# Optimization experiments

Hardware: AMD Instinct MI355X
Metric: run time of the kernel (lower is better)

Reference implementation:

```python
import jax, jax.numpy as jnp
import numpy as np

N, E, F_IN, H, C = 20000, 320000, 256, 4, 64
D = H * C  # hidden_dim = 256
NEG_SLOPE = 0.2
LN_EPS = 1e-5


def setup_inputs() -> dict:
    key = jax.random.key(0)
    ks = jax.random.split(key, 12)
    x = jax.random.normal(ks[0], (N, F_IN), dtype=jnp.float32)
    # edges guaranteed self-loop-free (PyG GATConv removes then re-adds self loops)
    dst = jax.random.randint(ks[1], (E,), 0, N)
    off = jax.random.randint(ks[2], (E,), 1, N)
    src = (dst + off) % N
    edge_index = jnp.stack([src, dst]).astype(jnp.int64)

    def lin(k, fan_in, shape):
        return jax.random.normal(k, shape, dtype=jnp.float32) / np.sqrt(fan_in)

    W1 = lin(ks[3], F_IN, (F_IN, D)); b1 = jnp.zeros((D,), jnp.float32)
    a_src1 = lin(ks[4], C, (H, C)); a_dst1 = lin(ks[5], C, (H, C))
    W2 = lin(ks[6], D, (D, D)); b2 = jnp.zeros((D,), jnp.float32)
    a_src2 = lin(ks[7], C, (H, C)); a_dst2 = lin(ks[8], C, (H, C))
    g1 = jnp.ones((D,), jnp.float32); be1 = jnp.zeros((D,), jnp.float32)
    g2 = jnp.ones((D,), jnp.float32); be2 = jnp.zeros((D,), jnp.float32)
    attn_w = lin(ks[9], D, (D, 1)); attn_b = jnp.zeros((1,), jnp.float32)
    return dict(x=x, edge_index=edge_index, W1=W1, b1=b1, a_src1=a_src1,
                a_dst1=a_dst1, W2=W2, b2=b2, a_src2=a_src2, a_dst2=a_dst2,
                g1=g1, be1=be1, g2=g2, be2=be2, attn_w=attn_w, attn_b=attn_b)


def _gat_conv(x, src, dst, W, b, a_src, a_dst):
    # x: [N, F] -> h: [N, H, C]
    h = (x @ W).reshape(N, H, C)
    alpha_s = jnp.einsum('nhc,hc->nh', h, a_src)  # [N, H]
    alpha_d = jnp.einsum('nhc,hc->nh', h, a_dst)
    e = jax.nn.leaky_relu(alpha_s[src] + alpha_d[dst], NEG_SLOPE)  # [E', H]
    # segment softmax over edges sharing a destination
    m = jax.ops.segment_max(e, dst, num_segments=N)
    w = jnp.exp(e - m[dst])
    z = jax.ops.segment_sum(w, dst, num_segments=N)
    alpha = w / (z[dst] + 1e-16)
    out = jax.ops.segment_sum(h[src] * alpha[:, :, None], dst, num_segments=N)
    return out.reshape(N, D) + b


def _layernorm(x, g, b):
    mu = x.mean(-1, keepdims=True)
    var = ((x - mu) ** 2).mean(-1, keepdims=True)
    return (x - mu) * jax.lax.rsqrt(var + LN_EPS) * g + b


def reference(x, edge_index, W1, b1, a_src1, a_dst1, W2, b2, a_src2, a_dst2,
              g1, be1, g2, be2, attn_w, attn_b):
    loops = jnp.arange(N, dtype=edge_index.dtype)
    src = jnp.concatenate([edge_index[0], loops])
    dst = jnp.concatenate([edge_index[1], loops])
    x1 = _gat_conv(x, src, dst, W1, b1, a_src1, a_dst1)
    x1 = jax.nn.elu(_layernorm(x1, g1, be1))
    x2 = _gat_conv(x1, src, dst, W2, b2, a_src2, a_dst2)
    x2 = jax.nn.elu(_layernorm(x2, g2, be2) + x1)
    attn = jax.nn.softmax(x2 @ attn_w + attn_b, axis=0)  # softmax over nodes
    pooled = (x2 * attn).sum(axis=0)  # [D]
    return pooled
```

## Files before the change

kernel.cpp:

```cpp
#include <hip/hip_runtime.h>
#include <math.h>

#define N_NODES 20000
#define E_EDGES 320000
#define TOT_E   (E_EDGES + N_NODES)
#define DHID    256
#define NHEAD   4
#define SCAN_NB ((N_NODES + 255) / 256)
#define SPART   32
#define ECAP    128
#define EB_K    ((TOT_E + 255) / 256)
#define XB_K    (N_NODES * 256 / 8 / 256)

typedef float f32x4 __attribute__((ext_vector_type(4)));
typedef short short8 __attribute__((ext_vector_type(8)));
typedef unsigned short ushort;

__device__ __forceinline__ float wave_sum(float v) {
#pragma unroll
  for (int off = 32; off; off >>= 1) v += __shfl_xor(v, off);
  return v;
}
__device__ __forceinline__ ushort f2bf(float f) {
  unsigned u = __float_as_uint(f);
  u += 0x7fffu + ((u >> 16) & 1u);
  return (ushort)(u >> 16);
}
__device__ __forceinline__ float bflo(unsigned u) {
  return __uint_as_float(u << 16);
}
__device__ __forceinline__ float bfhi(unsigned u) {
  return __uint_as_float(u & 0xffff0000u);
}

__global__ __launch_bounds__(256)
void conv_hist_kernel(const float* __restrict__ W1, const float* __restrict__ W2,
                      const float* __restrict__ x, const int* __restrict__ ei,
                      ushort* __restrict__ Wt1, ushort* __restrict__ Wt2,
                      ushort* __restrict__ xb, int* __restrict__ deg) {
  const int b = blockIdx.x;
  if (b < 512) {
    const float* W = (b < 256) ? W1 : W2;
    ushort* Wt = (b < 256) ? Wt1 : Wt2;
    const int n = b & 255;
    const int k = threadIdx.x;
    Wt[n * 256 + k] = f2bf(W[k * 256 + n]);
  } else if (b < 512 + XB_K) {
    int idx = (b - 512) * 256 + threadIdx.x;
    size_t base = (size_t)idx * 8;
    float4 a = *reinterpret_cast<const float4*>(x + base);
    float4 c = *reinterpret_cast<const float4*>(x + base + 4);
    short8 o;
    o[0] = f2bf(a.x); o[1] = f2bf(a.y); o[2] = f2bf(a.z); o[3] = f2bf(a.w);
    o[4] = f2bf(c.x); o[5] = f2bf(c.y); o[6] = f2bf(c.z); o[7] = f2bf(c.w);
    *reinterpret_cast<short8*>(xb + base) = o;
  } else {
    int e = (b - 512 - XB_K) * 256 + threadIdx.x;
    if (e < TOT_E) {
      int dst = (e < E_EDGES) ? ei[E_EDGES + e] : (e - E_EDGES);
      atomicAdd(&deg[dst], 1);
    }
  }
}

__global__ __launch_bounds__(256)
void scan_blocks_kernel(const int* __restrict__ deg, int* __restrict__ bsum) {
  __shared__ int ws[4];
  const int t = threadIdx.x;
  const int i = blockIdx.x * 256 + t;
  int v = (i < N_NODES) ? deg[i] : 0;
  int s = v;
#pragma unroll
  for (int off = 32; off; off >>= 1) s += __shfl_xor(s, off);
  if ((t & 63) == 0) ws[t >> 6] = s;
  __syncthreads();
  if (t == 0) bsum[blockIdx.x] = ws[0] + ws[1] + ws[2] + ws[3];
}

__global__ __launch_bounds__(256)
void scan_apply_kernel(const int* __restrict__ deg, const int* __restrict__ bsum,
                       int* __restrict__ rowp, int* __restrict__ cur) {
  __shared__ int ws[4], ws2[4];
  const int t = threadIdx.x;
  const int lane = t & 63, w = t >> 6;
  int part = 0;
  for (int k = t; k < blockIdx.x; k += 256) part += bsum[k];
#pragma unroll
  for (int off = 32; off; off >>= 1) part += __shfl_xor(part, off);
  if (lane == 0) ws[w] = part;
  __syncthreads();
  const int boff = ws[0] + ws[1] + ws[2] + ws[3];
  const int i = blockIdx.x * 256 + t;
  int v = (i < N_NODES) ? deg[i] : 0;
  int inc = v;
#pragma unroll
  for (int off = 1; off < 64; off <<= 1) {
    int u = __shfl_up(inc, off);
    if (lane >= off) inc += u;
  }
  if (lane == 63) ws2[w] = inc;
  __syncthreads();
  int add = boff;
#pragma unroll
  for (int k = 0; k < 4; ++k)
    if (k < w) add += ws2[k];
  int exc = add + inc - v;
  if (i < N_NODES) {
    rowp[i] = exc;
    cur[i] = exc;
    if (i == N_NODES - 1) rowp[N_NODES] = exc + v;
  }
}

__global__ void scatter_kernel(const int* __restrict__ ei, int* __restrict__ cur,
                               int* __restrict__ colb) {
  int e = blockIdx.x * blockDim.x + threadIdx.x;
  if (e >= TOT_E) return;
  int src, dst;
  if (e < E_EDGES) { src = ei[e]; dst = ei[E_EDGES + e]; }
  else             { src = dst = e - E_EDGES; }
  int pos = atomicAdd(&cur[dst], 1);
  colb[pos] = src;
}

__global__ __launch_bounds__(256)
void gemm_alpha_kernel(const ushort* __restrict__ Ab, const ushort* __restrict__ Wt,
                       const float* __restrict__ asrc, const float* __restrict__ adst,
                       ushort* __restrict__ hout, float* __restrict__ as_,
                       float* __restrict__ ad_) {
  __shared__ ushort hs[32 * 256];

  const int t = threadIdx.x;
  const int w = t >> 6;
  const int l = t & 63;
  const int row0 = blockIdx.x * 32;

  const ushort* abase = Ab + (size_t)(row0 + (l & 15)) * 256 + ((l >> 4) * 8);
  const ushort* bbase = Wt + (size_t)(w * 64 + (l & 15)) * 256 + ((l >> 4) * 8);

  f32x4 acc[2][4];
#pragma unroll
  for (int i = 0; i < 2; ++i)
#pragma unroll
    for (int j = 0; j < 4; ++j) acc[i][j] = (f32x4){0.f, 0.f, 0.f, 0.f};

  short8 a0 = *reinterpret_cast<const short8*>(abase);
  short8 a1 = *reinterpret_cast<const short8*>(abase + 16 * 256);
  short8 b0 = *reinterpret_cast<const short8*>(bbase);
  short8 b1 = *reinterpret_cast<const short8*>(bbase + 16 * 256);
  short8 b2 = *reinterpret_cast<const short8*>(bbase + 32 * 256);
  short8 b3 = *reinterpret_cast<const short8*>(bbase + 48 * 256);
#pragma unroll
  for (int kk = 0; kk < 256; kk += 32) {
    short8 na0, na1, nb0, nb1, nb2, nb3;
    if (kk + 32 < 256) {
      na0 = *reinterpret_cast<const short8*>(abase + kk + 32);
      na1 = *reinterpret_cast<const short8*>(abase + 16 * 256 + kk + 32);
      nb0 = *reinterpret_cast<const short8*>(bbase + kk + 32);
      nb1 = *reinterpret_cast<const short8*>(bbase + 16 * 256 + kk + 32);
      nb2 = *reinterpret_cast<const short8*>(bbase + 32 * 256 + kk + 32);
      nb3 = *reinterpret_cast<const short8*>(bbase + 48 * 256 + kk + 32);
    }
    acc[0][0] = __builtin_amdgcn_mfma_f32_16x16x32_bf16(a0, b0, acc[0][0], 0, 0, 0);
    acc[0][1] = __builtin_amdgcn_mfma_f32_16x16x32_bf16(a0, b1, acc[0][1], 0, 0, 0);
    acc[0][2] = __builtin_amdgcn_mfma_f32_16x16x32_bf16(a0, b2, acc[0][2], 0, 0, 0);
    acc[0][3] = __builtin_amdgcn_mfma_f32_16x16x32_bf16(a0, b3, acc[0][3], 0, 0, 0);
    acc[1][0] = __builtin_amdgcn_mfma_f32_16x16x32_bf16(a1, b0, acc[1][0], 0, 0, 0);
    acc[1][1] = __builtin_amdgcn_mfma_f32_16x16x32_bf16(a1, b1, acc[1][1], 0, 0, 0);
    acc[1][2] = __builtin_amdgcn_mfma_f32_16x16x32_bf16(a1, b2, acc[1][2], 0, 0, 0);
    acc[1][3] = __builtin_amdgcn_mfma_f32_16x16x32_bf16(a1, b3, acc[1][3], 0, 0, 0);
    if (kk + 32 < 256) {
      a0 = na0; a1 = na1; b0 = nb0; b1 = nb1; b2 = nb2; b3 = nb3;
    }
  }

  float asj[4], adj[4];
#pragma unroll
  for (int j = 0; j < 4; ++j) {
    asj[j] = asrc[w * 64 + j * 16 + (l & 15)];
    adj[j] = adst[w * 64 + j * 16 + (l & 15)];
  }
#pragma unroll
  for (int i = 0; i < 2; ++i) {
#pragma unroll
    for (int q = 0; q < 4; ++q) {
      float ps = 0.f, pd = 0.f;
#pragma unroll
      for (int j = 0; j < 4; ++j) {
        ps += acc[i][j][q] * asj[j];
        pd += acc[i][j][q] * adj[j];
      }
#pragma unroll
      for (int off = 1; off < 16; off <<= 1) {
        ps += __shfl_xor(ps, off);
        pd += __shfl_xor(pd, off);
      }
      int row = row0 + i * 16 + (l >> 4) * 4 + q;
      if ((l & 15) == 0) {
        as_[row * 4 + w] = ps;
        ad_[row * 4 + w] = pd;
      }
    }
  }

#pragma unroll
  for (int i = 0; i < 2; ++i)
#pragma unroll
    for (int j = 0; j < 4; ++j)
#pragma unroll
      for (int q = 0; q < 4; ++q) {
        int row = i * 16 + (l >> 4) * 4 + q;
        int col = w * 64 + j * 16 + (l & 15);
        hs[row * 256 + col] = f2bf(acc[i][j][q]);
      }
  __syncthreads();
#pragma unroll
  for (int g = 0; g < 4; ++g) {
    int gi = g * 256 + t;
    int row = gi >> 5;
    int slot = gi & 31;
    *reinterpret_cast<short8*>(hout + (size_t)(row0 + row) * 256 + slot * 8) =
        *reinterpret_cast<const short8*>(&hs[row * 256 + slot * 8]);
  }
}

__global__ __launch_bounds__(256)
void attn_gather_ln_kernel(const ushort* __restrict__ h, const float* __restrict__ as_,
                           const float* __restrict__ ad_, const int* __restrict__ rowp,
                           const int* __restrict__ colb, const float* __restrict__ bias,
                           const float* __restrict__ gamma, const float* __restrict__ beta,
                           const ushort* __restrict__ residb, ushort* __restrict__ outb,
                           const float* __restrict__ aw, const float* __restrict__ ab,
                           float* __restrict__ score) {
  __shared__ float ew[4][ECAP][NHEAD];
  __shared__ int   sidx[4][ECAP];

  const int t = threadIdx.x;
  const int wd = t >> 6;
  const int d = blockIdx.x * 4 + wd;
  const int l = t & 63;
  const int start = rowp[d];
  const int deg = rowp[d + 1] - start;
  const int* cb = colb + start;

  const int e16 = l >> 2, hh = l & 3;
  const float adv = ad_[d * 4 + hh];
  const int gh = l >> 4;
  const int c0 = l * 4;
  const ushort* hrow = h + c0;

  float zpart = 0.f;
  float a0 = 0.f, a1 = 0.f, a2 = 0.f, a3 = 0.f;

  for (int base = 0; base < deg; base += ECAP) {
    const int cnt = min(deg - base, ECAP);
    for (int i = e16; i < cnt; i += 16) {
      int s = cb[base + i];
      if (hh == 0) sidx[wd][i] = s;
      float e = as_[s * 4 + hh] + adv;
      e = (e >= 0.f) ? e : 0.2f * e;
      e = fminf(e, 60.f);
      float wv = __expf(e);
      ew[wd][i][hh] = wv;
      zpart += wv;
    }
    int i = 0;
    for (; i + 8 <= cnt; i += 8) {
      int ss[8]; float ww[8]; uint2 hv[8];
#pragma unroll
      for (int k = 0; k < 8; ++k) { ss[k] = sidx[wd][i + k]; ww[k] = ew[wd][i + k][gh]; }
#pragma unroll
      for (int k = 0; k < 8; ++k)
        hv[k] = *reinterpret_cast<const uint2*>(hrow + (size_t)ss[k] * 256);
#pragma unroll
      for (int k = 0; k < 8; ++k) {
        a0 += ww[k] * bflo(hv[k].x); a1 += ww[k] * bfhi(hv[k].x);
        a2 += ww[k] * bflo(hv[k].y); a3 += ww[k] * bfhi(hv[k].y);
      }
    }
    for (; i + 4 <= cnt; i += 4) {
      int ss[4]; float ww[4]; uint2 hv[4];
#pragma unroll
      for (int k = 0; k < 4; ++k) { ss[k] = sidx[wd][i + k]; ww[k] = ew[wd][i + k][gh]; }
#pragma unroll
      for (int k = 0; k < 4; ++k)
        hv[k] = *reinterpret_cast<const uint2*>(hrow + (size_t)ss[k] * 256);
#pragma unroll
      for (int k = 0; k < 4; ++k) {
        a0 += ww[k] * bflo(hv[k].x); a1 += ww[k] * bfhi(hv[k].x);
        a2 += ww[k] * bflo(hv[k].y); a3 += ww[k] * bfhi(hv[k].y);
      }
    }
    for (; i < cnt; ++i) {
      int s = sidx[wd][i];
      float wv = ew[wd][i][gh];
      uint2 hv = *reinterpret_cast<const uint2*>(hrow + (size_t)s * 256);
      a0 += wv * bflo(hv.x);
      a1 += wv * bfhi(hv.x);
      a2 += wv * bflo(hv.y);
      a3 += wv * bfhi(hv.y);
    }
  }

#pragma unroll
  for (int off = 4; off < 64; off <<= 1) zpart += __shfl_xor(zpart, off);
  const float zi = 1.f / (__shfl(zpart, gh) + 1e-16f);

  float4 bi = *reinterpret_cast<const float4*>(bias + c0);
  float v0 = a0 * zi + bi.x, v1 = a1 * zi + bi.y;
  float v2 = a2 * zi + bi.z, v3 = a3 * zi + bi.w;

  float s1 = wave_sum(v0 + v1 + v2 + v3);
  float s2 = wave_sum(v0 * v0 + v1 * v1 + v2 * v2 + v3 * v3);
  float mu = s1 * (1.f / 256.f);
  float var = s2 * (1.f / 256.f) - mu * mu;
  float rstd = rsqrtf(var + 1e-5f);
  float4 ga = *reinterpret_cast<const float4*>(gamma + c0);
  float4 be = *reinterpret_cast<const float4*>(beta + c0);
  float y0 = (v0 - mu) * rstd * ga.x + be.x;
  float y1 = (v1 - mu) * rstd * ga.y + be.y;
  float y2 = (v2 - mu) * rstd * ga.z + be.z;
  float y3 = (v3 - mu) * rstd * ga.w + be.w;
  if (residb) {
    uint2 rv = *reinterpret_cast<const uint2*>(residb + (size_t)d * 256 + c0);
    y0 += bflo(rv.x); y1 += bfhi(rv.x); y2 += bflo(rv.y); y3 += bfhi(rv.y);
  }
  y0 = (y0 > 0.f) ? y0 : expm1f(y0);
  y1 = (y1 > 0.f) ? y1 : expm1f(y1);
  y2 = (y2 > 0.f) ? y2 : expm1f(y2);
  y3 = (y3 > 0.f) ? y3 : expm1f(y3);

  uint2 o;
  o.x = ((unsigned)f2bf(y0)) | (((unsigned)f2bf(y1)) << 16);
  o.y = ((unsigned)f2bf(y2)) | (((unsigned)f2bf(y3)) << 16);
  *reinterpret_cast<uint2*>(outb + (size_t)d * 256 + c0) = o;

  if (score) {
    float4 aww = *reinterpret_cast<const float4*>(aw + c0);
    float sp = wave_sum(y0 * aww.x + y1 * aww.y + y2 * aww.z + y3 * aww.w);
    if (l == 0) score[d] = sp + ab[0];
  }
}

__global__ __launch_bounds__(256)
void score_part_kernel(const float* __restrict__ s, float* __restrict__ pm,
                       float* __restrict__ pz) {
  __shared__ float red[4];
  const int t = threadIdx.x, b = blockIdx.x;
  const int lane = t & 63, wid = t >> 6;
  float m = -INFINITY;
  for (int n = b * 256 + t; n < N_NODES; n += SPART * 256) m = fmaxf(m, s[n]);
#pragma unroll
  for (int off = 32; off; off >>= 1) m = fmaxf(m, __shfl_xor(m, off));
  if (lane == 0) red[wid] = m;
  __syncthreads();
  m = fmaxf(fmaxf(red[0], red[1]), fmaxf(red[2], red[3]));
  __syncthreads();
  float z = 0.f;
  for (int n = b * 256 + t; n < N_NODES; n += SPART * 256) z += __expf(s[n] - m);
  z = wave_sum(z);
  if (lane == 0) red[wid] = z;
  __syncthreads();
  if (t == 0) { pm[b] = m; pz[b] = red[0] + red[1] + red[2] + red[3]; }
}

__global__ __launch_bounds__(64)
void score_comb_kernel(const float* __restrict__ pm, const float* __restrict__ pz,
                       float* __restrict__ mz) {
  const int l = threadIdx.x;
  float m = (l < SPART) ? pm[l] : -INFINITY;
#pragma unroll
  for (int off = 32; off; off >>= 1) m = fmaxf(m, __shfl_xor(m, off));
  float z = (l < SPART) ? pz[l] * __expf(pm[l] - m) : 0.f;
  z = wave_sum(z);
  if (l == 0) { mz[0] = m; mz[1] = z; }
}

__global__ __launch_bounds__(256)
void pool_partial_kernel(const ushort* __restrict__ hb2, const float* __restrict__ s,
                         const float* __restrict__ mz, float* __restrict__ part) {
  __shared__ float red4[4][256];
  const int t = threadIdx.x, b = blockIdx.x;
  const int c4 = t & 63, rsub = t >> 6;
  const float m = mz[0];
  const float invz = 1.f / mz[1];
  f32x4 acc = (f32x4){0.f, 0.f, 0.f, 0.f};
  for (int n = b * 4 + rsub; n < N_NODES; n += 1024) {
    float w = __expf(s[n] - m);
    uint2 hv = *reinterpret_cast<const uint2*>(hb2 + (size_t)n * 256 + c4 * 4);
    acc[0] += w * bflo(hv.x);
    acc[1] += w * bfhi(hv.x);
    acc[2] += w * bflo(hv.y);
    acc[3] += w * bfhi(hv.y);
  }
#pragma unroll
  for (int k = 0; k < 4; ++k) red4[rsub][c4 * 4 + k] = acc[k];
  __syncthreads();
  if (t < 256) {
    float v = red4[0][t] + red4[1][t] + red4[2][t] + red4[3][t];
    part[b * 256 + t] = v * invz;
  }
}

__global__ __launch_bounds__(256)
void pool_final_kernel(const float* __restrict__ part, float* __restrict__ out) {
  const int t = threadIdx.x;
  float acc = 0.f;
  for (int b = 0; b < 256; ++b) acc += part[b * 256 + t];
  out[t] = acc;
}

extern "C" void kernel_launch(void* const* d_in, const int* in_sizes, int n_in,
                              void* d_out, int out_size, void* d_ws, size_t ws_size,
                              hipStream_t stream) {
  const float* x      = (const float*)d_in[0];
  const int*   ei     = (const int*)d_in[1];
  const float* W1     = (const float*)d_in[2];
  const float* b1     = (const float*)d_in[3];
  const float* a_src1 = (const float*)d_in[4];
  const float* a_dst1 = (const float*)d_in[5];
  const float* W2     = (const float*)d_in[6];
  const float* b2     = (const float*)d_in[7];
  const float* a_src2 = (const float*)d_in[8];
  const float* a_dst2 = (const float*)d_in[9];
  const float* g1     = (const float*)d_in[10];
  const float* be1    = (const float*)d_in[11];
  const float* g2     = (const float*)d_in[12];
  const float* be2    = (const float*)d_in[13];
  const float* attn_w = (const float*)d_in[14];
  const float* attn_b = (const float*)d_in[15];
  float* out = (float*)d_out;

  char* p = (char*)d_ws;
  auto alloc = [&](size_t bytes) {
    char* r = p;
    p += (bytes + 255) & ~size_t(255);
    return r;
  };
  ushort* h   = (ushort*)alloc((size_t)N_NODES * 256 * 2);
  ushort* xb  = (ushort*)alloc((size_t)N_NODES * 256 * 2);
  ushort* xb1 = (ushort*)alloc((size_t)N_NODES * 256 * 2);
  ushort* hb2 = (ushort*)alloc((size_t)N_NODES * 256 * 2);
  float* as_  = (float*)alloc((size_t)N_NODES * 4 * 4);
  float* ad_  = (float*)alloc((size_t)N_NODES * 4 * 4);
  float* sbuf = (float*)alloc((size_t)N_NODES * 4);
  float* mz   = (float*)alloc(256);
  float* pm   = (float*)alloc((size_t)SPART * 4);
  float* pz   = (float*)alloc((size_t)SPART * 4);
  float* part = (float*)alloc((size_t)256 * 256 * 4);
  ushort* wt1 = (ushort*)alloc((size_t)256 * 256 * 2);
  ushort* wt2 = (ushort*)alloc((size_t)256 * 256 * 2);
  int* deg    = (int*)alloc((size_t)N_NODES * 4);
  int* rowp   = (int*)alloc((size_t)(N_NODES + 1) * 4);
  int* cur    = (int*)alloc((size_t)N_NODES * 4);
  int* colb   = (int*)alloc((size_t)TOT_E * 4);
  int* bsum   = (int*)alloc((size_t)SCAN_NB * 4);

  const int GB = N_NODES / 32;
  const int DB = N_NODES / 4;
  const int CONVB = 512 + XB_K + EB_K;

  hipMemsetAsync(deg, 0, (size_t)N_NODES * 4, stream);
  conv_hist_kernel<<<CONVB, 256, 0, stream>>>(W1, W2, x, ei, wt1, wt2, xb, deg);
  scan_blocks_kernel<<<SCAN_NB, 256, 0, stream>>>(deg, bsum);
  scan_apply_kernel<<<SCAN_NB, 256, 0, stream>>>(deg, bsum, rowp, cur);
  scatter_kernel<<<EB_K, 256, 0, stream>>>(ei, cur, colb);

  gemm_alpha_kernel<<<GB, 256, 0, stream>>>(xb, wt1, a_src1, a_dst1, h, as_, ad_);
  attn_gather_ln_kernel<<<DB, 256, 0, stream>>>(h, as_, ad_, rowp, colb, b1, g1, be1,
                                                nullptr, xb1, nullptr, nullptr, nullptr);
  gemm_alpha_kernel<<<GB, 256, 0, stream>>>(xb1, wt2, a_src2, a_dst2, h, as_, ad_);
  attn_gather_ln_kernel<<<DB, 256, 0, stream>>>(h, as_, ad_, rowp, colb, b2, g2, be2,
                                                xb1, hb2, attn_w, attn_b, sbuf);
  score_part_kernel<<<SPART, 256, 0, stream>>>(sbuf, pm, pz);
  score_comb_kernel<<<1, 64, 0, stream>>>(pm, pz, mz);
  pool_partial_kernel<<<256, 256, 0, stream>>>(hb2, sbuf, mz, part);
  pool_final_kernel<<<1, 256, 0, stream>>>(part, out);
}
```

Measured before the change: 173.0 us.

## Prescale gather offsets, raise wave priority in gather loop, fuse score combine into pool

The gather kernel now stores source indices pre-shifted into byte offsets in shared memory, which removes the per-edge multiply from the address calculation. It also raises wave priority with s_setprio around the gather loop so waves issuing loads get scheduled first. The separate single-block score_comb kernel is removed; each pool_partial block recomputes the global max and normalizer from the 32 partials, which saves one launch at the cost of redundant tiny work in every block. The shifted offset s<<9 stays within int range for 20000 nodes.

```diff
diff --git a/kernel.cpp b/kernel.cpp
--- a/kernel.cpp
+++ b/kernel.cpp
@@ -247,7 +247,7 @@
   const float adv = ad_[d * 4 + hh];
   const int gh = l >> 4;
   const int c0 = l * 4;
-  const ushort* hrow = h + c0;
+  const char* hrow = reinterpret_cast<const char*>(h + c0);
 
   float zpart = 0.f;
   float a0 = 0.f, a1 = 0.f, a2 = 0.f, a3 = 0.f;
@@ -256,7 +256,7 @@
     const int cnt = min(deg - base, ECAP);
     for (int i = e16; i < cnt; i += 16) {
       int s = cb[base + i];
-      if (hh == 0) sidx[wd][i] = s;
+      if (hh == 0) sidx[wd][i] = s << 9;
       float e = as_[s * 4 + hh] + adv;
       e = (e >= 0.f) ? e : 0.2f * e;
       e = fminf(e, 60.f);
@@ -264,6 +264,7 @@
       ew[wd][i][hh] = wv;
       zpart += wv;
     }
+    __builtin_amdgcn_s_setprio(1);
     int i = 0;
     for (; i + 8 <= cnt; i += 8) {
       int ss[8]; float ww[8]; uint2 hv[8];
@@ -271,7 +272,7 @@
       for (int k = 0; k < 8; ++k) { ss[k] = sidx[wd][i + k]; ww[k] = ew[wd][i + k][gh]; }
 #pragma unroll
       for (int k = 0; k < 8; ++k)
-        hv[k] = *reinterpret_cast<const uint2*>(hrow + (size_t)ss[k] * 256);
+        hv[k] = *reinterpret_cast<const uint2*>(hrow + (size_t)ss[k]);
 #pragma unroll
       for (int k = 0; k < 8; ++k) {
         a0 += ww[k] * bflo(hv[k].x); a1 += ww[k] * bfhi(hv[k].x);
@@ -284,7 +285,7 @@
       for (int k = 0; k < 4; ++k) { ss[k] = sidx[wd][i + k]; ww[k] = ew[wd][i + k][gh]; }
 #pragma unroll
       for (int k = 0; k < 4; ++k)
-        hv[k] = *reinterpret_cast<const uint2*>(hrow + (size_t)ss[k] * 256);
+        hv[k] = *reinterpret_cast<const uint2*>(hrow + (size_t)ss[k]);
 #pragma unroll
       for (int k = 0; k < 4; ++k) {
         a0 += ww[k] * bflo(hv[k].x); a1 += ww[k] * bfhi(hv[k].x);
@@ -292,14 +293,15 @@
       }
     }
     for (; i < cnt; ++i) {
-      int s = sidx[wd][i];
+      int soff = sidx[wd][i];
       float wv = ew[wd][i][gh];
-      uint2 hv = *reinterpret_cast<const uint2*>(hrow + (size_t)s * 256);
+      uint2 hv = *reinterpret_cast<const uint2*>(hrow + (size_t)soff);
       a0 += wv * bflo(hv.x);
       a1 += wv * bfhi(hv.x);
       a2 += wv * bflo(hv.y);
       a3 += wv * bfhi(hv.y);
     }
+    __builtin_amdgcn_s_setprio(0);
   }
 
 #pragma unroll
@@ -364,26 +366,25 @@
   if (t == 0) { pm[b] = m; pz[b] = red[0] + red[1] + red[2] + red[3]; }
 }
 
-__global__ __launch_bounds__(64)
-void score_comb_kernel(const float* __restrict__ pm, const float* __restrict__ pz,
-                       float* __restrict__ mz) {
-  const int l = threadIdx.x;
-  float m = (l < SPART) ? pm[l] : -INFINITY;
-#pragma unroll
-  for (int off = 32; off; off >>= 1) m = fmaxf(m, __shfl_xor(m, off));
-  float z = (l < SPART) ? pz[l] * __expf(pm[l] - m) : 0.f;
-  z = wave_sum(z);
-  if (l == 0) { mz[0] = m; mz[1] = z; }
-}
-
 __global__ __launch_bounds__(256)
 void pool_partial_kernel(const ushort* __restrict__ hb2, const float* __restrict__ s,
-                         const float* __restrict__ mz, float* __restrict__ part) {
+                         const float* __restrict__ pm, const float* __restrict__ pz,
+                         float* __restrict__ part) {
   __shared__ float red4[4][256];
+  __shared__ float sMZ[2];
   const int t = threadIdx.x, b = blockIdx.x;
   const int c4 = t & 63, rsub = t >> 6;
-  const float m = mz[0];
-  const float invz = 1.f / mz[1];
+  if (t < 64) {
+    float m = (t < SPART) ? pm[t] : -INFINITY;
+#pragma unroll
+    for (int off = 32; off; off >>= 1) m = fmaxf(m, __shfl_xor(m, off));
+    float z = (t < SPART) ? pz[t] * __expf(pm[t] - m) : 0.f;
+    z = wave_sum(z);
+    if (t == 0) { sMZ[0] = m; sMZ[1] = z; }
+  }
+  __syncthreads();
+  const float m = sMZ[0];
+  const float invz = 1.f / sMZ[1];
   f32x4 acc = (f32x4){0.f, 0.f, 0.f, 0.f};
   for (int n = b * 4 + rsub; n < N_NODES; n += 1024) {
     float w = __expf(s[n] - m);
@@ -444,7 +445,6 @@
   float* as_  = (float*)alloc((size_t)N_NODES * 4 * 4);
   float* ad_  = (float*)alloc((size_t)N_NODES * 4 * 4);
   float* sbuf = (float*)alloc((size_t)N_NODES * 4);
-  float* mz   = (float*)alloc(256);
   float* pm   = (float*)alloc((size_t)SPART * 4);
   float* pz   = (float*)alloc((size_t)SPART * 4);
   float* part = (float*)alloc((size_t)256 * 256 * 4);
@@ -473,7 +473,6 @@
   attn_gather_ln_kernel<<<DB, 256, 0, stream>>>(h, as_, ad_, rowp, colb, b2, g2, be2,
                                                 xb1, hb2, attn_w, attn_b, sbuf);
   score_part_kernel<<<SPART, 256, 0, stream>>>(sbuf, pm, pz);
-  score_comb_kernel<<<1, 64, 0, stream>>>(pm, pz, mz);
-  pool_partial_kernel<<<256, 256, 0, stream>>>(hb2, sbuf, mz, part);
+  pool_partial_kernel<<<256, 256, 0, stream>>>(hb2, sbuf, pm, pz, part);
   pool_final_kernel<<<1, 256, 0, stream>>>(part, out);
 }
```

Result: no change. 174.2 us (+0.7%).
